# Kernel optimization log

Measured on AMD Instinct MI355X. Metric: run time of the kernel, lower is better.

The kernel has to match this reference:

```python
import jax, jax.numpy as jnp
import numpy as np

OUT, IN = 11008, 4096
B, S = 8, 32


def setup_inputs() -> dict:
    key = jax.random.key(0)
    k_x, k_w, k_s, k_b = jax.random.split(key, 4)
    x = jax.random.normal(k_x, (B, S, IN), dtype=jnp.float32).astype(jnp.float16)
    # int8 weight storage (symmetric quant range [-128, 127])
    w_int8 = jax.random.randint(k_w, (OUT, IN), -128, 128, dtype=jnp.int32).astype(jnp.int8)
    # per-output-channel scale, small positive values typical of int8 quant
    scale = jax.random.uniform(k_s, (OUT,), dtype=jnp.float32) * 0.01 + 1e-4
    bias = (jax.random.normal(k_b, (OUT,), dtype=jnp.float32) * 0.02).astype(jnp.float16)
    return {"x": x, "w_int8": w_int8, "scale": scale, "bias": bias}


def reference(x, w_int8, scale, bias):
    # w_fp[o, i] = int8_weight[o, i] * scale[o]   (on-the-fly dequant)
    w = w_int8.astype(jnp.float32) * scale[:, None]          # [OUT, IN] fp32
    # F.linear: out = x @ w.T + bias, computed in fp32
    out = jnp.einsum('bsi,oi->bso', x.astype(jnp.float32), w) + bias.astype(jnp.float32)
    return out.astype(x.dtype)                                # cast back to x.dtype (fp16)
```

## Files before the change

### kernel.cpp

```cpp
#include <hip/hip_runtime.h>
#include <hip/hip_bf16.h>
#include <stdint.h>

typedef __attribute__((ext_vector_type(8))) __bf16 bf16x8;
typedef __attribute__((ext_vector_type(4))) float f32x4;

constexpr int K_DIM = 4096;
constexpr int N_DIM = 11008;
constexpr int M_DIM = 256;
constexpr int TM = 256;
constexpr int TN = 64;
constexpr int BK = 64;
constexpr int NT = 512;
constexpr int KT_ALL = K_DIM / BK;
constexpr int KSPLIT = 3;

__device__ __forceinline__ void gload_lds16(const __bf16* gptr, __bf16* lptr) {
  __builtin_amdgcn_global_load_lds(
      (const __attribute__((address_space(1))) uint32_t*)gptr,
      (__attribute__((address_space(3))) uint32_t*)lptr, 16, 0, 0);
}

__device__ __forceinline__ bf16x8 cvt8f(const float4 u0, const float4 u1) {
  bf16x8 v;
  v[0] = (__bf16)u0.x; v[1] = (__bf16)u0.y; v[2] = (__bf16)u0.z; v[3] = (__bf16)u0.w;
  v[4] = (__bf16)u1.x; v[5] = (__bf16)u1.y; v[6] = (__bf16)u1.z; v[7] = (__bf16)u1.w;
  return v;
}
__device__ __forceinline__ bf16x8 cvt8i(const int4 a, const int4 b) {
  bf16x8 v;
  v[0] = (__bf16)(float)a.x; v[1] = (__bf16)(float)a.y;
  v[2] = (__bf16)(float)a.z; v[3] = (__bf16)(float)a.w;
  v[4] = (__bf16)(float)b.x; v[5] = (__bf16)(float)b.y;
  v[6] = (__bf16)(float)b.z; v[7] = (__bf16)(float)b.w;
  return v;
}

__global__ void cvt_x_kernel(const float* __restrict__ x, __bf16* __restrict__ ws) {
  const int i = (blockIdx.x * 256 + threadIdx.x) * 8;
  const float4 u0 = ((const float4*)(x + i))[0];
  const float4 u1 = ((const float4*)(x + i))[1];
  *(bf16x8*)(ws + i) = cvt8f(u0, u1);
}

__global__ void cvt_w_kernel(const int* __restrict__ w, __bf16* __restrict__ wbf) {
  const size_t i = ((size_t)blockIdx.x * 256 + threadIdx.x) * 8;
  const int4 a = ((const int4*)(w + i))[0];
  const int4 b = ((const int4*)(w + i))[1];
  *(bf16x8*)(wbf + i) = cvt8i(a, b);
}

template<bool A_WS, bool W_WS>
__global__ __launch_bounds__(NT, 4) void int8_linear_kernel(
    const float* __restrict__ x,
    const __bf16* __restrict__ xws,
    const int*   __restrict__ w,
    const __bf16* __restrict__ wbf,
    const float* __restrict__ scale,
    const float* __restrict__ bias,
    float*       __restrict__ out)
{
  __shared__ __bf16 As[2][TM * BK];
  __shared__ __bf16 Wsh[2][TN * BK];

  const int tid  = threadIdx.x;
  const int lane = tid & 63;
  const int wv   = tid >> 6;
  const int quad = lane >> 4;
  const int l16  = lane & 15;
  const int m_base = (wv >> 1) * 64;
  const int wn     = wv & 1;
  const int n_base = blockIdx.x * TN;
  const int kc     = blockIdx.y;

  const int t0 = (kc * KT_ALL) / KSPLIT;
  const int t1 = ((kc + 1) * KT_ALL) / KSPLIT;
  const int ntile = t1 - t0;

  f32x4 acc[4][2];
#pragma unroll
  for (int i = 0; i < 4; ++i)
#pragma unroll
    for (int j = 0; j < 2; ++j) acc[i][j] = (f32x4){0.f, 0.f, 0.f, 0.f};

  auto stage = [&](int t, int buf) {
    const int kt = t0 + t;
    if (A_WS) {
#pragma unroll
      for (int j = 0; j < 4; ++j) {
        const int c = j * 512 + tid;
        const int row = c >> 3;
        const int k8 = (c & 7) ^ (row & 7);
        gload_lds16(xws + (int64_t)row * K_DIM + kt * BK + k8 * 8, As[buf] + c * 8);
      }
    } else {
#pragma unroll
      for (int j = 0; j < 4; ++j) {
        const int c = j * 512 + tid;
        const int row = c >> 3;
        const int k8 = c & 7;
        const float* s = x + (int64_t)row * K_DIM + kt * BK + k8 * 8;
        const bf16x8 v = cvt8f(((const float4*)s)[0], ((const float4*)s)[1]);
        *(bf16x8*)(As[buf] + row * BK + (k8 ^ (row & 7)) * 8) = v;
      }
    }
    const int row = tid >> 3;
    const int k8l = tid & 7;
    if (W_WS) {
      const int k8 = k8l ^ (row & 7);
      gload_lds16(wbf + (int64_t)(n_base + row) * K_DIM + kt * BK + k8 * 8,
                  Wsh[buf] + tid * 8);
    } else {
      const int4* p = (const int4*)(w + (int64_t)(n_base + row) * K_DIM + kt * BK + k8l * 8);
      const bf16x8 v = cvt8i(p[0], p[1]);
      *(bf16x8*)(Wsh[buf] + row * BK + (k8l ^ (row & 7)) * 8) = v;
    }
  };
  auto compute = [&](const __bf16* abuf, const __bf16* wbuf) {
#pragma unroll
    for (int ks = 0; ks < 2; ++ks) {
      bf16x8 a[4], b[2];
#pragma unroll
      for (int mi = 0; mi < 4; ++mi) {
        const int m = m_base + mi * 16 + l16;
        const int slot = (ks * 4 + quad) ^ (m & 7);
        a[mi] = *(const bf16x8*)(abuf + m * BK + slot * 8);
      }
#pragma unroll
      for (int ni = 0; ni < 2; ++ni) {
        const int n = wn * 32 + ni * 16 + l16;
        const int slot = (ks * 4 + quad) ^ (n & 7);
        b[ni] = *(const bf16x8*)(wbuf + n * BK + slot * 8);
      }
#pragma unroll
      for (int mi = 0; mi < 4; ++mi)
#pragma unroll
        for (int ni = 0; ni < 2; ++ni)
          acc[mi][ni] = __builtin_amdgcn_mfma_f32_16x16x32_bf16(
              a[mi], b[ni], acc[mi][ni], 0, 0, 0);
    }
  };

  stage(0, 0);
  __syncthreads();
  for (int t = 0; t < ntile; ++t) {
    if (t + 1 < ntile) stage(t + 1, (t + 1) & 1);
    compute(As[t & 1], Wsh[t & 1]);
    __syncthreads();
  }

#pragma unroll
  for (int ni = 0; ni < 2; ++ni) {
    const int col = n_base + wn * 32 + ni * 16 + l16;
    const float sc = scale[col];
    const float bi = (kc == 0) ? bias[col] : 0.0f;
#pragma unroll
    for (int mi = 0; mi < 4; ++mi) {
      const int row0 = m_base + mi * 16 + quad * 4;
#pragma unroll
      for (int r = 0; r < 4; ++r)
        unsafeAtomicAdd(out + (int64_t)(row0 + r) * N_DIM + col,
                        acc[mi][ni][r] * sc + bi);
    }
  }
}

extern "C" void kernel_launch(void* const* d_in, const int* in_sizes, int n_in,
                              void* d_out, int out_size, void* d_ws, size_t ws_size,
                              hipStream_t stream) {
  const float* x     = (const float*)d_in[0];
  const int*   w     = (const int*)d_in[1];
  const float* scale = (const float*)d_in[2];
  const float* bias  = (const float*)d_in[3];
  float* out = (float*)d_out;

  const size_t xws_bytes = (size_t)M_DIM * K_DIM * sizeof(__bf16);
  const size_t wbf_bytes = (size_t)N_DIM * K_DIM * sizeof(__bf16);
  __bf16* xws = (__bf16*)d_ws;
  __bf16* wbf = (__bf16*)((char*)d_ws + xws_bytes);

  hipMemsetAsync(out, 0, (size_t)M_DIM * N_DIM * sizeof(float), stream);

  dim3 grid(N_DIM / TN, KSPLIT), block(NT);
  if (ws_size >= xws_bytes + wbf_bytes) {
    cvt_x_kernel<<<M_DIM * K_DIM / 2048, 256, 0, stream>>>(x, xws);
    cvt_w_kernel<<<(int)(((size_t)N_DIM * K_DIM) / 2048), 256, 0, stream>>>(w, wbf);
    int8_linear_kernel<true, true><<<grid, block, 0, stream>>>(
        x, xws, w, wbf, scale, bias, out);
  } else if (ws_size >= xws_bytes) {
    cvt_x_kernel<<<M_DIM * K_DIM / 2048, 256, 0, stream>>>(x, xws);
    int8_linear_kernel<true, false><<<grid, block, 0, stream>>>(
        x, xws, w, wbf, scale, bias, out);
  } else {
    int8_linear_kernel<false, false><<<grid, block, 0, stream>>>(
        x, xws, w, wbf, scale, bias, out);
  }
}
```

Before: 339.9 us.

## Pack int32 weights to tiled int8 and dequantize in registers inside GEMM

Replaces the bf16 weight conversion pass with a pass that packs the int32-stored weights into a tile-contiguous int8 buffer. The GEMM then loads 8 bytes per thread per tile, converts to bf16 in registers and writes to LDS after the MFMA compute, overlapping global loads with compute. This cuts the bytes written by the pre-pass and read by the GEMM for weights. The cost is extra VALU unpacking work in the GEMM and loss of the direct global-to-LDS path for weights.

```diff
diff --git a/kernel.cpp b/kernel.cpp
--- a/kernel.cpp
+++ b/kernel.cpp
@@ -14,6 +14,7 @@
 constexpr int NT = 512;
 constexpr int KT_ALL = K_DIM / BK;
 constexpr int KSPLIT = 3;
+constexpr int WTILE = TN * BK;
 
 __device__ __forceinline__ void gload_lds16(const __bf16* gptr, __bf16* lptr) {
   __builtin_amdgcn_global_load_lds(
@@ -43,19 +44,32 @@
   *(bf16x8*)(ws + i) = cvt8f(u0, u1);
 }
 
-__global__ void cvt_w_kernel(const int* __restrict__ w, __bf16* __restrict__ wbf) {
-  const size_t i = ((size_t)blockIdx.x * 256 + threadIdx.x) * 8;
-  const int4 a = ((const int4*)(w + i))[0];
-  const int4 b = ((const int4*)(w + i))[1];
-  *(bf16x8*)(wbf + i) = cvt8i(a, b);
-}
-
-template<bool A_WS, bool W_WS>
+__global__ void pack_w_kernel(const int* __restrict__ w, int8_t* __restrict__ wp) {
+  const int j = blockIdx.x * 256 + threadIdx.x;
+  const int e = j * 32;
+  const int tile = e >> 12;
+  const int o = e & 4095;
+  const int wrow = o >> 6;
+  const int col0 = o & 63;
+  const int nb = tile >> 6, kt = tile & 63;
+  const int4* src = (const int4*)(w + (int64_t)(nb * 64 + wrow) * K_DIM + kt * 64 + col0);
+  int pk[8];
+#pragma unroll
+  for (int q = 0; q < 8; ++q) {
+    const int4 a = src[q];
+    pk[q] = (a.x & 0xFF) | ((a.y & 0xFF) << 8) | ((a.z & 0xFF) << 16) | (a.w << 24);
+  }
+  int4* dst = (int4*)(wp + (size_t)e);
+  dst[0] = make_int4(pk[0], pk[1], pk[2], pk[3]);
+  dst[1] = make_int4(pk[4], pk[5], pk[6], pk[7]);
+}
+
+template<bool A_WS, bool W_PK>
 __global__ __launch_bounds__(NT, 4) void int8_linear_kernel(
     const float* __restrict__ x,
     const __bf16* __restrict__ xws,
     const int*   __restrict__ w,
-    const __bf16* __restrict__ wbf,
+    const int8_t* __restrict__ wp,
     const float* __restrict__ scale,
     const float* __restrict__ bias,
     float*       __restrict__ out)
@@ -70,20 +84,50 @@
   const int l16  = lane & 15;
   const int m_base = (wv >> 1) * 64;
   const int wn     = wv & 1;
-  const int n_base = blockIdx.x * TN;
+  const int nb     = blockIdx.x;
+  const int n_base = nb * TN;
   const int kc     = blockIdx.y;
 
   const int t0 = (kc * KT_ALL) / KSPLIT;
   const int t1 = ((kc + 1) * KT_ALL) / KSPLIT;
   const int ntile = t1 - t0;
 
+  const int wrow   = tid >> 3;
+  const int wchunk = tid & 7;
+  const int wslot  = wchunk ^ (wrow & 7);
+
   f32x4 acc[4][2];
 #pragma unroll
   for (int i = 0; i < 4; ++i)
 #pragma unroll
     for (int j = 0; j < 2; ++j) acc[i][j] = (f32x4){0.f, 0.f, 0.f, 0.f};
 
-  auto stage = [&](int t, int buf) {
+  uint2 pw;
+  int4  wi0, wi1;
+  auto wload = [&](int t) {
+    if (W_PK) {
+      pw = *(const uint2*)(wp + (size_t)(nb * KT_ALL + t0 + t) * WTILE + tid * 8);
+    } else {
+      const int4* p = (const int4*)(w + (int64_t)(n_base + wrow) * K_DIM +
+                                    (t0 + t) * BK + wchunk * 8);
+      wi0 = p[0]; wi1 = p[1];
+    }
+  };
+  auto commitW = [&](__bf16* wbuf) {
+    bf16x8 v;
+    if (W_PK) {
+#pragma unroll
+      for (int e = 0; e < 4; ++e)
+        v[e] = (__bf16)(float)(int)(int8_t)((pw.x >> (8 * e)) & 0xFF);
+#pragma unroll
+      for (int e = 0; e < 4; ++e)
+        v[4 + e] = (__bf16)(float)(int)(int8_t)((pw.y >> (8 * e)) & 0xFF);
+    } else {
+      v = cvt8i(wi0, wi1);
+    }
+    *(bf16x8*)(wbuf + wrow * BK + wslot * 8) = v;
+  };
+  auto a_stage = [&](int t, __bf16* abuf) {
     const int kt = t0 + t;
     if (A_WS) {
 #pragma unroll
@@ -91,7 +135,7 @@
         const int c = j * 512 + tid;
         const int row = c >> 3;
         const int k8 = (c & 7) ^ (row & 7);
-        gload_lds16(xws + (int64_t)row * K_DIM + kt * BK + k8 * 8, As[buf] + c * 8);
+        gload_lds16(xws + (int64_t)row * K_DIM + kt * BK + k8 * 8, abuf + c * 8);
       }
     } else {
 #pragma unroll
@@ -100,20 +144,9 @@
         const int row = c >> 3;
         const int k8 = c & 7;
         const float* s = x + (int64_t)row * K_DIM + kt * BK + k8 * 8;
-        const bf16x8 v = cvt8f(((const float4*)s)[0], ((const float4*)s)[1]);
-        *(bf16x8*)(As[buf] + row * BK + (k8 ^ (row & 7)) * 8) = v;
-      }
-    }
-    const int row = tid >> 3;
-    const int k8l = tid & 7;
-    if (W_WS) {
-      const int k8 = k8l ^ (row & 7);
-      gload_lds16(wbf + (int64_t)(n_base + row) * K_DIM + kt * BK + k8 * 8,
-                  Wsh[buf] + tid * 8);
-    } else {
-      const int4* p = (const int4*)(w + (int64_t)(n_base + row) * K_DIM + kt * BK + k8l * 8);
-      const bf16x8 v = cvt8i(p[0], p[1]);
-      *(bf16x8*)(Wsh[buf] + row * BK + (k8l ^ (row & 7)) * 8) = v;
+        const bf16x8 vv = cvt8f(((const float4*)s)[0], ((const float4*)s)[1]);
+        *(bf16x8*)(abuf + row * BK + (k8 ^ (row & 7)) * 8) = vv;
+      }
     }
   };
   auto compute = [&](const __bf16* abuf, const __bf16* wbuf) {
@@ -141,11 +174,17 @@
     }
   };
 
-  stage(0, 0);
+  wload(0);
+  commitW(Wsh[0]);
+  a_stage(0, As[0]);
   __syncthreads();
+
   for (int t = 0; t < ntile; ++t) {
-    if (t + 1 < ntile) stage(t + 1, (t + 1) & 1);
+    const int nxt = (t + 1) & 1;
+    const bool more = (t + 1 < ntile);
+    if (more) { wload(t + 1); a_stage(t + 1, As[nxt]); }
     compute(As[t & 1], Wsh[t & 1]);
+    if (more) commitW(Wsh[nxt]);
     __syncthreads();
   }
 
@@ -175,24 +214,24 @@
   float* out = (float*)d_out;
 
   const size_t xws_bytes = (size_t)M_DIM * K_DIM * sizeof(__bf16);
-  const size_t wbf_bytes = (size_t)N_DIM * K_DIM * sizeof(__bf16);
+  const size_t wp_bytes  = (size_t)N_DIM * K_DIM;
   __bf16* xws = (__bf16*)d_ws;
-  __bf16* wbf = (__bf16*)((char*)d_ws + xws_bytes);
+  int8_t* wpp = (int8_t*)((char*)d_ws + xws_bytes);
 
   hipMemsetAsync(out, 0, (size_t)M_DIM * N_DIM * sizeof(float), stream);
 
   dim3 grid(N_DIM / TN, KSPLIT), block(NT);
-  if (ws_size >= xws_bytes + wbf_bytes) {
+  if (ws_size >= xws_bytes + wp_bytes) {
     cvt_x_kernel<<<M_DIM * K_DIM / 2048, 256, 0, stream>>>(x, xws);
-    cvt_w_kernel<<<(int)(((size_t)N_DIM * K_DIM) / 2048), 256, 0, stream>>>(w, wbf);
+    pack_w_kernel<<<(int)(((size_t)N_DIM * K_DIM / 32) / 256), 256, 0, stream>>>(w, wpp);
     int8_linear_kernel<true, true><<<grid, block, 0, stream>>>(
-        x, xws, w, wbf, scale, bias, out);
+        x, xws, w, wpp, scale, bias, out);
   } else if (ws_size >= xws_bytes) {
     cvt_x_kernel<<<M_DIM * K_DIM / 2048, 256, 0, stream>>>(x, xws);
     int8_linear_kernel<true, false><<<grid, block, 0, stream>>>(
-        x, xws, w, wbf, scale, bias, out);
+        x, xws, w, wpp, scale, bias, out);
   } else {
     int8_linear_kernel<false, false><<<grid, block, 0, stream>>>(
-        x, xws, w, wbf, scale, bias, out);
-  }
-}
+        x, xws, w, wpp, scale, bias, out);
+  }
+}
```

Measured after the change: 339.2 us. About the same (-0.2%).
